# Kernel optimization log

Hardware: AMD Instinct MI355X
Metric: run time of the kernel (lower is better)

The kernel has to match this reference:

```python
import jax, jax.numpy as jnp
import numpy as np

OUT_FEATURES = 4096
IN_FEATURES = 4096
NNZ = 1677722
BATCH, SEQ = 2, 2048


def setup_inputs() -> dict:
    key = jax.random.key(0)
    k1, k2, k3, k4 = jax.random.split(key, 4)
    x = jax.random.normal(k1, (BATCH, SEQ, IN_FEATURES), dtype=jnp.float32)
    data = jax.random.normal(k2, (NNZ,), dtype=jnp.float32)
    rows = jax.random.randint(k3, (NNZ,), 0, OUT_FEATURES, dtype=jnp.int32)
    cols = jax.random.randint(k4, (NNZ,), 0, IN_FEATURES, dtype=jnp.int32)
    return {"x": x, "data": data, "rows": rows, "cols": cols}


def reference(x, data, rows, cols):
    # Densify sparse weight W [out_features, in_features] from COO triples
    # (equivalent math to the CSR spmm in the original module).
    W = jnp.zeros((OUT_FEATURES, IN_FEATURES), dtype=data.dtype)
    W = W.at[rows, cols].add(data)
    # Original: (W @ x_flat.T).T reshaped -> y = x @ W^T, shape [B, S, out]
    return jnp.einsum("bsi,oi->bso", x, W)
```

## Files before the change

### kernel.cpp

```cpp
#include <hip/hip_runtime.h>
#include <stdint.h>

#define M_ROWS 4096
#define N_OUT  4096
#define K_IN   4096
#define NNZ_N  1677722
#define CAP    640
#define NB     256
#define BCHUNK 6656

typedef __attribute__((ext_vector_type(8))) short  bf16x8_t;
typedef __attribute__((ext_vector_type(4))) float  f32x4_t;

__device__ __forceinline__ unsigned short f2bf(float f) {
    union { float f; uint32_t u; } v; v.f = f;
    uint32_t u = v.u;
    u += 0x7FFFu + ((u >> 16) & 1u);
    return (unsigned short)(u >> 16);
}

__global__ void convert_x(const float4* __restrict__ x, uint4* __restrict__ xo) {
    int i = blockIdx.x * blockDim.x + threadIdx.x;
    float4 a = x[2 * i], b = x[2 * i + 1];
    uint4 o;
    o.x = (uint32_t)f2bf(a.x) | ((uint32_t)f2bf(a.y) << 16);
    o.y = (uint32_t)f2bf(a.z) | ((uint32_t)f2bf(a.w) << 16);
    o.z = (uint32_t)f2bf(b.x) | ((uint32_t)f2bf(b.y) << 16);
    o.w = (uint32_t)f2bf(b.z) | ((uint32_t)f2bf(b.w) << 16);
    xo[i] = o;
}

__global__ __launch_bounds__(1024) void hist_coo(const int* __restrict__ rows,
                                                 uint32_t* __restrict__ Hist) {
    __shared__ uint32_t h[N_OUT];
    const int blk = blockIdx.x, t = threadIdx.x;
    for (int j = t; j < N_OUT; j += 1024) h[j] = 0;
    __syncthreads();
    const int start = blk * BCHUNK;
    const int end   = min(start + BCHUNK, NNZ_N);
    for (int i = start + t; i < end; i += 1024)
        atomicAdd(&h[rows[i]], 1u);
    __syncthreads();
    for (int j = t; j < N_OUT; j += 1024)
        Hist[(size_t)blk * N_OUT + j] = h[j];
}

__global__ __launch_bounds__(256) void scan_hist(uint32_t* __restrict__ Hist,
                                                 uint32_t* __restrict__ cnt) {
    const int bin  = blockIdx.x * 4 + (threadIdx.x >> 6);
    const int lane = threadIdx.x & 63;
    uint32_t v[4], pre[4];
#pragma unroll
    for (int q = 0; q < 4; ++q)
        v[q] = Hist[(size_t)(lane * 4 + q) * N_OUT + bin];
    pre[0] = 0;
#pragma unroll
    for (int q = 1; q < 4; ++q) pre[q] = pre[q - 1] + v[q - 1];
    uint32_t tot = pre[3] + v[3];
    uint32_t x = tot;
#pragma unroll
    for (int off = 1; off < 64; off <<= 1) {
        uint32_t y = __shfl_up(x, off);
        if (lane >= off) x += y;
    }
    uint32_t excl = x - tot;
#pragma unroll
    for (int q = 0; q < 4; ++q)
        Hist[(size_t)(lane * 4 + q) * N_OUT + bin] = excl + pre[q];
    if (lane == 63) cnt[bin] = excl + tot;
}

__global__ __launch_bounds__(1024) void place_coo(const float* __restrict__ data,
                                                  const int* __restrict__ rows,
                                                  const int* __restrict__ cols,
                                                  const uint32_t* __restrict__ Base,
                                                  uint32_t* __restrict__ bucket) {
    __shared__ uint32_t cur[N_OUT];
    const int blk = blockIdx.x, t = threadIdx.x;
    for (int j = t; j < N_OUT; j += 1024)
        cur[j] = Base[(size_t)blk * N_OUT + j];
    __syncthreads();
    const int start = blk * BCHUNK;
    const int end   = min(start + BCHUNK, NNZ_N);
    for (int i = start + t; i < end; i += 1024) {
        int r = rows[i];
        uint32_t slot = atomicAdd(&cur[r], 1u);
        if (slot < CAP)
            bucket[(size_t)r * CAP + slot] =
                ((uint32_t)cols[i] << 16) | (uint32_t)f2bf(data[i]);
    }
}

__global__ __launch_bounds__(256) void accum_rows(const uint32_t* __restrict__ cnt,
                                                  const uint32_t* __restrict__ bucket,
                                                  unsigned short* __restrict__ W) {
    __shared__ float acc[K_IN];
    const int r = blockIdx.x;
    const int t = threadIdx.x;

    float4* av = (float4*)acc;
#pragma unroll
    for (int j = t; j < K_IN / 4; j += 256) av[j] = (float4){0.f, 0.f, 0.f, 0.f};
    __syncthreads();

    uint32_t n = cnt[r];
    if (n > CAP) n = CAP;
    const uint32_t* b = bucket + (size_t)r * CAP;
    for (uint32_t j = t; j < n; j += 256) {
        uint32_t e = b[j];
        union { uint32_t u; float f; } v; v.u = (e & 0xFFFFu) << 16;
        atomicAdd(&acc[e >> 16], v.f);
    }
    __syncthreads();

    uint4* wv = (uint4*)(W + (size_t)r * K_IN);
#pragma unroll
    for (int j = t; j < K_IN / 8; j += 256) {
        float4 a = av[2 * j], c = av[2 * j + 1];
        uint4 o;
        o.x = (uint32_t)f2bf(a.x) | ((uint32_t)f2bf(a.y) << 16);
        o.y = (uint32_t)f2bf(a.z) | ((uint32_t)f2bf(a.w) << 16);
        o.z = (uint32_t)f2bf(c.x) | ((uint32_t)f2bf(c.y) << 16);
        o.w = (uint32_t)f2bf(c.z) | ((uint32_t)f2bf(c.w) << 16);
        wv[j] = o;
    }
}

__device__ __forceinline__ void async_ld16(const void* g, void* lds_wave_base) {
    __builtin_amdgcn_global_load_lds(
        (const __attribute__((address_space(1))) uint32_t*)g,
        (__attribute__((address_space(3))) uint32_t*)lds_wave_base,
        16, 0, 0);
}

#define STAGE_M(gbase, lbase, kt, slot) do {                                   \
    const unsigned short* g_ = (gbase) + (kt) * 64;                            \
    unsigned short*       l_ = (lbase) + (slot) * 32768;                       \
    async_ld16(g_,                  l_);                                       \
    async_ld16(g_ + 1 * 64 * K_IN,  l_ + 4096);                                \
    async_ld16(g_ + 2 * 64 * K_IN,  l_ + 8192);                                \
    async_ld16(g_ + 3 * 64 * K_IN,  l_ + 12288);                               \
} while (0)

__global__ __launch_bounds__(512, 2) void gemm_bt(const unsigned short* __restrict__ A,
                                                  const unsigned short* __restrict__ B,
                                                  float* __restrict__ C) {
    __shared__ __align__(16) unsigned short lds_[65536];

    const int t    = threadIdx.x;
    const int wave = t >> 6;
    const int lane = t & 63;
    const int wr   = wave >> 2;
    const int wc   = wave & 3;
    const int m0   = blockIdx.y * 256;
    const int n0   = blockIdx.x * 256;

    const int srow = t >> 3;
    const int sch  = ((t & 7) ^ (srow & 7)) * 8;
    const unsigned short* gA = A + (size_t)(m0 + srow) * K_IN + sch;
    const unsigned short* gB = B + (size_t)(n0 + srow) * K_IN + sch;
    unsigned short* lA = lds_ + wave * 512;
    unsigned short* lB = lds_ + 16384 + wave * 512;

    const int l15  = lane & 15;
    const int aoff = (wr * 128 + l15) * 64;
    const int boff = (wc * 64  + l15) * 64;
    const int ck0  = (((lane >> 4)    ) ^ (lane & 7)) * 8;
    const int ck1  = (((lane >> 4) | 4) ^ (lane & 7)) * 8;

    f32x4_t acc[8][4];
#pragma unroll
    for (int i = 0; i < 8; ++i)
#pragma unroll
        for (int j = 0; j < 4; ++j) acc[i][j] = (f32x4_t){0.f, 0.f, 0.f, 0.f};

    bf16x8_t af[4][2], bf0[2][2], bf1[2][2];

    STAGE_M(gA, lA, 0, 0); STAGE_M(gB, lB, 0, 0);
    STAGE_M(gA, lA, 1, 1); STAGE_M(gB, lB, 1, 1);
    asm volatile("s_waitcnt vmcnt(8)" ::: "memory");
    __builtin_amdgcn_s_barrier();

    for (int kt = 0; kt < 64; ++kt) {
        const unsigned short* pA = lds_ + (kt & 1) * 32768;
        const unsigned short* pB = pA + 16384;

#pragma unroll
        for (int im = 0; im < 4; ++im) {
            af[im][0] = *(const bf16x8_t*)(pA + aoff + im * 1024 + ck0);
            af[im][1] = *(const bf16x8_t*)(pA + aoff + im * 1024 + ck1);
        }
#pragma unroll
        for (int jn = 0; jn < 2; ++jn) {
            bf0[jn][0] = *(const bf16x8_t*)(pB + boff + jn * 1024 + ck0);
            bf0[jn][1] = *(const bf16x8_t*)(pB + boff + jn * 1024 + ck1);
        }
        __builtin_amdgcn_s_barrier();
        asm volatile("s_waitcnt lgkmcnt(0)" ::: "memory");
        __builtin_amdgcn_s_setprio(1);
#pragma unroll
        for (int im = 0; im < 4; ++im)
#pragma unroll
            for (int jn = 0; jn < 2; ++jn)
#pragma unroll
                for (int kk = 0; kk < 2; ++kk)
                    acc[im][jn] = __builtin_amdgcn_mfma_f32_16x16x32_bf16(
                        af[im][kk], bf0[jn][kk], acc[im][jn], 0, 0, 0);
        __builtin_amdgcn_s_setprio(0);
        __builtin_amdgcn_s_barrier();

#pragma unroll
        for (int jn = 0; jn < 2; ++jn) {
            bf1[jn][0] = *(const bf16x8_t*)(pB + boff + (2 + jn) * 1024 + ck0);
            bf1[jn][1] = *(const bf16x8_t*)(pB + boff + (2 + jn) * 1024 + ck1);
        }
        __builtin_amdgcn_s_barrier();
        asm volatile("s_waitcnt lgkmcnt(0)" ::: "memory");
        __builtin_amdgcn_s_setprio(1);
#pragma unroll
        for (int im = 0; im < 4; ++im)
#pragma unroll
            for (int jn = 0; jn < 2; ++jn)
#pragma unroll
                for (int kk = 0; kk < 2; ++kk)
                    acc[im][2 + jn] = __builtin_amdgcn_mfma_f32_16x16x32_bf16(
                        af[im][kk], bf1[jn][kk], acc[im][2 + jn], 0, 0, 0);
        __builtin_amdgcn_s_setprio(0);
        __builtin_amdgcn_s_barrier();

        if (kt < 62) STAGE_M(gB, lB, kt + 2, (kt & 1));
#pragma unroll
        for (int im = 0; im < 4; ++im) {
            af[im][0] = *(const bf16x8_t*)(pA + aoff + (4 + im) * 1024 + ck0);
            af[im][1] = *(const bf16x8_t*)(pA + aoff + (4 + im) * 1024 + ck1);
        }
        __builtin_amdgcn_s_barrier();
        asm volatile("s_waitcnt lgkmcnt(0)" ::: "memory");
        __builtin_amdgcn_s_setprio(1);
#pragma unroll
        for (int im = 0; im < 4; ++im)
#pragma unroll
            for (int jn = 0; jn < 2; ++jn)
#pragma unroll
                for (int kk = 0; kk < 2; ++kk)
                    acc[4 + im][jn] = __builtin_amdgcn_mfma_f32_16x16x32_bf16(
                        af[im][kk], bf0[jn][kk], acc[4 + im][jn], 0, 0, 0);
        __builtin_amdgcn_s_setprio(0);
        __builtin_amdgcn_s_barrier();

        if (kt < 62) STAGE_M(gA, lA, kt + 2, (kt & 1));
        __builtin_amdgcn_s_setprio(1);
#pragma unroll
        for (int im = 0; im < 4; ++im)
#pragma unroll
            for (int jn = 0; jn < 2; ++jn)
#pragma unroll
                for (int kk = 0; kk < 2; ++kk)
                    acc[4 + im][2 + jn] = __builtin_amdgcn_mfma_f32_16x16x32_bf16(
                        af[im][kk], bf1[jn][kk], acc[4 + im][2 + jn], 0, 0, 0);
        __builtin_amdgcn_s_setprio(0);
        if (kt < 62) {
            asm volatile("s_waitcnt vmcnt(8)" ::: "memory");
        } else {
            asm volatile("s_waitcnt vmcnt(0)" ::: "memory");
        }
        __builtin_amdgcn_s_barrier();
    }

    const int crow = m0 + wr * 128 + ((lane >> 4) << 2);
    const int ccol = n0 + wc * 64 + l15;
#pragma unroll
    for (int im = 0; im < 8; ++im)
#pragma unroll
        for (int jn = 0; jn < 4; ++jn)
#pragma unroll
            for (int r = 0; r < 4; ++r)
                C[(size_t)(crow + im * 16 + r) * N_OUT + ccol + jn * 16] =
                    acc[im][jn][r];
}

extern "C" void kernel_launch(void* const* d_in, const int* in_sizes, int n_in,
                              void* d_out, int out_size, void* d_ws, size_t ws_size,
                              hipStream_t stream) {
    const float* x    = (const float*)d_in[0];
    const float* data = (const float*)d_in[1];
    const int*   rows = (const int*)d_in[2];
    const int*   cols = (const int*)d_in[3];
    float*       out  = (float*)d_out;

    unsigned short* W_bf16 = (unsigned short*)d_ws;
    unsigned short* x_bf16 = (unsigned short*)((char*)d_ws + (32u << 20));
    uint32_t*       Hist   = (uint32_t*)((char*)d_ws + (64u << 20));
    uint32_t*       cnt    = (uint32_t*)((char*)d_ws + (68u << 20));
    uint32_t*       bucket = (uint32_t*)((char*)d_ws + (69u << 20));

    convert_x<<<(M_ROWS * K_IN) / (8 * 256), 256, 0, stream>>>(
        (const float4*)x, (uint4*)x_bf16);

    hist_coo<<<NB, 1024, 0, stream>>>(rows, Hist);

    scan_hist<<<N_OUT / 4, 256, 0, stream>>>(Hist, cnt);

    place_coo<<<NB, 1024, 0, stream>>>(data, rows, cols, Hist, bucket);

    accum_rows<<<N_OUT, 256, 0, stream>>>(cnt, bucket, W_bf16);

    dim3 grid(N_OUT / 256, M_ROWS / 256);
    gemm_bt<<<grid, 512, 0, stream>>>(x_bf16, W_bf16, out);
}
```

Baseline: 316.4 us.

## Replace fixed-capacity row buckets with compact sorted run over 4-row bins

The COO-to-dense build now bins entries by groups of four output rows (1024 bins), scans per-block and global offsets, and does a local counting sort in LDS so each block writes its entries contiguously into a packed run array. This replaces the per-row fixed-capacity buckets (CAP=640), which wasted memory and scattered writes and silently dropped overflow entries. Each accumulation block now densifies four rows using a 64KB LDS accumulator with workgroup-scoped atomics. It adds an extra single-block scan kernel and heavier LDS use per block, which may lower occupancy.

```diff
diff --git a/kernel.cpp b/kernel.cpp
--- a/kernel.cpp
+++ b/kernel.cpp
@@ -5,9 +5,9 @@
 #define N_OUT  4096
 #define K_IN   4096
 #define NNZ_N  1677722
-#define CAP    640
-#define NB     256
-#define BCHUNK 6656
+#define NBLK   256
+#define CHUNK  6560
+#define NBINS  1024
 
 typedef __attribute__((ext_vector_type(8))) short  bf16x8_t;
 typedef __attribute__((ext_vector_type(4))) float  f32x4_t;
@@ -30,29 +30,29 @@
     xo[i] = o;
 }
 
-__global__ __launch_bounds__(1024) void hist_coo(const int* __restrict__ rows,
-                                                 uint32_t* __restrict__ Hist) {
-    __shared__ uint32_t h[N_OUT];
+__global__ __launch_bounds__(512) void hist_coo(const int* __restrict__ rows,
+                                                uint32_t* __restrict__ Hist) {
+    __shared__ uint32_t h[NBINS];
     const int blk = blockIdx.x, t = threadIdx.x;
-    for (int j = t; j < N_OUT; j += 1024) h[j] = 0;
-    __syncthreads();
-    const int start = blk * BCHUNK;
-    const int end   = min(start + BCHUNK, NNZ_N);
-    for (int i = start + t; i < end; i += 1024)
-        atomicAdd(&h[rows[i]], 1u);
-    __syncthreads();
-    for (int j = t; j < N_OUT; j += 1024)
-        Hist[(size_t)blk * N_OUT + j] = h[j];
-}
-
-__global__ __launch_bounds__(256) void scan_hist(uint32_t* __restrict__ Hist,
-                                                 uint32_t* __restrict__ cnt) {
+    for (int j = t; j < NBINS; j += 512) h[j] = 0;
+    __syncthreads();
+    const int start = blk * CHUNK;
+    const int end   = (start + CHUNK < NNZ_N) ? start + CHUNK : NNZ_N;
+    for (int i = start + t; i < end; i += 512)
+        atomicAdd(&h[rows[i] >> 2], 1u);
+    __syncthreads();
+    for (int j = t; j < NBINS; j += 512)
+        Hist[(size_t)blk * NBINS + j] = h[j];
+}
+
+__global__ __launch_bounds__(256) void scan_blocks(uint32_t* __restrict__ Hist,
+                                                   uint32_t* __restrict__ cnt) {
     const int bin  = blockIdx.x * 4 + (threadIdx.x >> 6);
     const int lane = threadIdx.x & 63;
     uint32_t v[4], pre[4];
 #pragma unroll
     for (int q = 0; q < 4; ++q)
-        v[q] = Hist[(size_t)(lane * 4 + q) * N_OUT + bin];
+        v[q] = Hist[(size_t)(lane * 4 + q) * NBINS + bin];
     pre[0] = 0;
 #pragma unroll
     for (int q = 1; q < 4; ++q) pre[q] = pre[q - 1] + v[q - 1];
@@ -66,56 +66,100 @@
     uint32_t excl = x - tot;
 #pragma unroll
     for (int q = 0; q < 4; ++q)
-        Hist[(size_t)(lane * 4 + q) * N_OUT + bin] = excl + pre[q];
+        Hist[(size_t)(lane * 4 + q) * NBINS + bin] = excl + pre[q];
     if (lane == 63) cnt[bin] = excl + tot;
 }
 
-__global__ __launch_bounds__(1024) void place_coo(const float* __restrict__ data,
-                                                  const int* __restrict__ rows,
-                                                  const int* __restrict__ cols,
-                                                  const uint32_t* __restrict__ Base,
-                                                  uint32_t* __restrict__ bucket) {
-    __shared__ uint32_t cur[N_OUT];
+__global__ __launch_bounds__(1024) void scan_tot(const uint32_t* __restrict__ cnt,
+                                                 uint32_t* __restrict__ Btot) {
+    __shared__ uint32_t s[NBINS];
+    const int t = threadIdx.x;
+    uint32_t v = cnt[t];
+    s[t] = v;
+    __syncthreads();
+    for (int off = 1; off < NBINS; off <<= 1) {
+        uint32_t a = (t >= off) ? s[t - off] : 0u;
+        __syncthreads();
+        s[t] += a;
+        __syncthreads();
+    }
+    Btot[t] = s[t] - v;
+    if (t == NBINS - 1) Btot[NBINS] = s[t];
+}
+
+__global__ __launch_bounds__(512) void place_coo(const float* __restrict__ data,
+                                                 const int* __restrict__ rows,
+                                                 const int* __restrict__ cols,
+                                                 const uint32_t* __restrict__ Base,
+                                                 const uint32_t* __restrict__ Btot,
+                                                 uint32_t* __restrict__ run) {
+    __shared__ uint32_t hist2[NBINS], basev[NBINS], curv[NBINS], gbase[NBINS];
+    __shared__ uint32_t ebuf[CHUNK];
+    __shared__ uint16_t binof[CHUNK];
     const int blk = blockIdx.x, t = threadIdx.x;
-    for (int j = t; j < N_OUT; j += 1024)
-        cur[j] = Base[(size_t)blk * N_OUT + j];
-    __syncthreads();
-    const int start = blk * BCHUNK;
-    const int end   = min(start + BCHUNK, NNZ_N);
-    for (int i = start + t; i < end; i += 1024) {
+    const int start = blk * CHUNK;
+    const int end   = (start + CHUNK < NNZ_N) ? start + CHUNK : NNZ_N;
+    const int nloc  = end - start;
+
+    for (int j = t; j < NBINS; j += 512) {
+        hist2[j] = 0;
+        gbase[j] = Btot[j] + Base[(size_t)blk * NBINS + j];
+    }
+    __syncthreads();
+    for (int i = start + t; i < end; i += 512)
+        atomicAdd(&hist2[rows[i] >> 2], 1u);
+    __syncthreads();
+    if (t < 64) {
+        uint32_t pre[16], loc = 0;
+#pragma unroll
+        for (int q = 0; q < 16; ++q) { pre[q] = loc; loc += hist2[t * 16 + q]; }
+        uint32_t xv = loc;
+#pragma unroll
+        for (int off = 1; off < 64; off <<= 1) {
+            uint32_t y = __shfl_up(xv, off);
+            if (t >= off) xv += y;
+        }
+        uint32_t excl = xv - loc;
+#pragma unroll
+        for (int q = 0; q < 16; ++q) {
+            basev[t * 16 + q] = excl + pre[q];
+            curv[t * 16 + q]  = excl + pre[q];
+        }
+    }
+    __syncthreads();
+    for (int i = start + t; i < end; i += 512) {
         int r = rows[i];
-        uint32_t slot = atomicAdd(&cur[r], 1u);
-        if (slot < CAP)
-            bucket[(size_t)r * CAP + slot] =
-                ((uint32_t)cols[i] << 16) | (uint32_t)f2bf(data[i]);
-    }
-}
-
-__global__ __launch_bounds__(256) void accum_rows(const uint32_t* __restrict__ cnt,
-                                                  const uint32_t* __restrict__ bucket,
+        uint32_t slot = atomicAdd(&curv[r >> 2], 1u);
+        ebuf[slot]  = ((uint32_t)(r & 3) << 28) |
+                      ((uint32_t)cols[i] << 16) | (uint32_t)f2bf(data[i]);
+        binof[slot] = (uint16_t)(r >> 2);
+    }
+    __syncthreads();
+    for (int j = t; j < nloc; j += 512) {
+        uint32_t b = binof[j];
+        run[gbase[b] + (j - basev[b])] = ebuf[j];
+    }
+}
+
+__global__ __launch_bounds__(512) void accum_bins(const uint32_t* __restrict__ run,
+                                                  const uint32_t* __restrict__ Btot,
                                                   unsigned short* __restrict__ W) {
-    __shared__ float acc[K_IN];
-    const int r = blockIdx.x;
-    const int t = threadIdx.x;
-
+    __shared__ float acc[4 * K_IN];
+    const int f = blockIdx.x, t = threadIdx.x;
     float4* av = (float4*)acc;
-#pragma unroll
-    for (int j = t; j < K_IN / 4; j += 256) av[j] = (float4){0.f, 0.f, 0.f, 0.f};
-    __syncthreads();
-
-    uint32_t n = cnt[r];
-    if (n > CAP) n = CAP;
-    const uint32_t* b = bucket + (size_t)r * CAP;
-    for (uint32_t j = t; j < n; j += 256) {
-        uint32_t e = b[j];
-        union { uint32_t u; float f; } v; v.u = (e & 0xFFFFu) << 16;
-        atomicAdd(&acc[e >> 16], v.f);
-    }
-    __syncthreads();
-
-    uint4* wv = (uint4*)(W + (size_t)r * K_IN);
-#pragma unroll
-    for (int j = t; j < K_IN / 8; j += 256) {
+    for (int j = t; j < 4 * K_IN / 4; j += 512) av[j] = (float4){0.f, 0.f, 0.f, 0.f};
+    __syncthreads();
+    const uint32_t s = Btot[f], e = Btot[f + 1];
+    for (uint32_t j = s + t; j < e; j += 512) {
+        uint32_t en = run[j];
+        union { uint32_t u; float fv; } v; v.u = (en & 0xFFFFu) << 16;
+        __hip_atomic_fetch_add(
+            &acc[((en >> 28) & 3u) * K_IN + ((en >> 16) & 0xFFFu)],
+            v.fv, __ATOMIC_RELAXED, __HIP_MEMORY_SCOPE_WORKGROUP);
+    }
+    __syncthreads();
+    uint4* wv = (uint4*)(W + (size_t)f * 4 * K_IN);
+    for (int j = t; j < 4 * K_IN / 8; j += 512) {
         float4 a = av[2 * j], c = av[2 * j + 1];
         uint4 o;
         o.x = (uint32_t)f2bf(a.x) | ((uint32_t)f2bf(a.y) << 16);
@@ -291,19 +335,21 @@
     unsigned short* W_bf16 = (unsigned short*)d_ws;
     unsigned short* x_bf16 = (unsigned short*)((char*)d_ws + (32u << 20));
     uint32_t*       Hist   = (uint32_t*)((char*)d_ws + (64u << 20));
-    uint32_t*       cnt    = (uint32_t*)((char*)d_ws + (68u << 20));
-    uint32_t*       bucket = (uint32_t*)((char*)d_ws + (69u << 20));
+    uint32_t*       cnt    = (uint32_t*)((char*)d_ws + (66u << 20));
+    uint32_t*       Btot   = (uint32_t*)((char*)d_ws + (66u << 20) + (64u << 10));
+    uint32_t*       run    = (uint32_t*)((char*)d_ws + (68u << 20));
 
     convert_x<<<(M_ROWS * K_IN) / (8 * 256), 256, 0, stream>>>(
         (const float4*)x, (uint4*)x_bf16);
 
-    hist_coo<<<NB, 1024, 0, stream>>>(rows, Hist);
-
-    scan_hist<<<N_OUT / 4, 256, 0, stream>>>(Hist, cnt);
-
-    place_coo<<<NB, 1024, 0, stream>>>(data, rows, cols, Hist, bucket);
-
-    accum_rows<<<N_OUT, 256, 0, stream>>>(cnt, bucket, W_bf16);
+    hist_coo<<<NBLK, 512, 0, stream>>>(rows, Hist);
+
+    scan_blocks<<<NBINS / 4, 256, 0, stream>>>(Hist, cnt);
+    scan_tot<<<1, NBINS, 0, stream>>>(cnt, Btot);
+
+    place_coo<<<NBLK, 512, 0, stream>>>(data, rows, cols, Hist, Btot, run);
+
+    accum_bins<<<NBINS, 512, 0, stream>>>(run, Btot, W_bf16);
 
     dim3 grid(N_OUT / 256, M_ROWS / 256);
     gemm_bt<<<grid, 512, 0, stream>>>(x_bf16, W_bf16, out);
```

After: 295.6 us. 1.07x faster.
